# Optimization experiments

Measured on AMD Instinct MI355X. Metric: run time of the kernel, lower is better.

## Reference

```python
import jax, jax.numpy as jnp
import numpy as np

VOCAB = 50257   # vocab_size
BASE = 64       # base_dim
DD = 64         # domain_dim (hidden width of each tiny domain MLP)
ND = 16         # number of grown domains (<= max_domains=30)
B, S = 16, 8192
CORR_SCALE = 0.1  # correction scale from forward()


def setup_inputs() -> dict:
    key = jax.random.key(0)
    k1, k2, k3, k4, k5 = jax.random.split(key, 5)
    x = jax.random.randint(k1, (B, S), 0, VOCAB)
    # token -> domain assignment; values >= ND mean "no domain" (~half assigned)
    token_domain = jax.random.randint(k2, (VOCAB,), 0, 2 * ND)
    base_embed = jax.random.normal(k3, (VOCAB, BASE), dtype=jnp.float32) * 0.02
    W1 = jax.random.normal(k4, (ND, BASE, DD), dtype=jnp.float32) * 0.01
    W2 = jax.random.normal(k5, (ND, DD, BASE), dtype=jnp.float32) * 0.01
    return {"x": x, "token_domain": token_domain,
            "base_embed": base_embed, "W1": W1, "W2": W2}


def reference(x, token_domain, base_embed, W1, W2):
    # h: [B, S, BASE] base embedding lookup
    h = base_embed[x]
    d = token_domain[x]  # [B, S] domain id per token; >= ND -> unassigned
    out = h
    # Loop over the small fixed set of domains (MoE-style combine).
    # Each domain: Linear(no bias) -> exact GELU -> Linear(no bias), scaled by 0.1,
    # added only where the token belongs to that domain.
    for i in range(ND):
        hid = jax.nn.gelu(jnp.einsum('bsc,cd->bsd', h, W1[i]), approximate=False)
        corr = jnp.einsum('bsd,dc->bsc', hid, W2[i])
        out = out + jnp.where((d == i)[..., None], CORR_SCALE * corr, 0.0)
    return out
```

## Files before the change

kernel.cpp:

```cpp
#include <hip/hip_runtime.h>
#include <hip/hip_bf16.h>

#define VOCABSZ 50257
#define BASEDIM 64
#define ND 16
#define NTOK (16 * 8192)
#define NBLK_PER_DOM 32

typedef __attribute__((ext_vector_type(8))) short short8;
typedef __attribute__((ext_vector_type(4))) float f32x4;

__device__ __forceinline__ short f2bf(float f) {
    union { float f; unsigned u; } v; v.f = f;
    unsigned r = (v.u + 0x7FFFu + ((v.u >> 16) & 1u)) >> 16;
    return (short)r;
}

__global__ __launch_bounds__(256) void k_bucket_base(
    const int* __restrict__ x, const int* __restrict__ tdom,
    const float* __restrict__ emb, float* __restrict__ out,
    int* __restrict__ g_cnt, int* __restrict__ bucket, int cap)
{
    __shared__ int sm_d[256];
    __shared__ int sm_x[256];
    __shared__ int sm_cnt[ND];
    __shared__ int sm_base[ND];

    const int lt = threadIdx.x;
    const int t0 = blockIdx.x * 256;
    const int t  = t0 + lt;

    if (lt < ND) sm_cnt[lt] = 0;
    __syncthreads();

    const int xt = x[t];
    const int d  = tdom[xt];
    sm_x[lt] = xt;
    sm_d[lt] = d;
    int pos = -1;
    if (d < ND) pos = atomicAdd(&sm_cnt[d], 1);
    __syncthreads();

    if (lt < ND) sm_base[lt] = atomicAdd(&g_cnt[lt], sm_cnt[lt]);
    __syncthreads();

    if (d < ND) {
        const int gp = sm_base[d] + pos;
        if (gp < cap) bucket[d * cap + gp] = t;
    }

    const int g = lt >> 4, l16 = lt & 15;
    const float4* embv = (const float4*)emb;
    float4* outv = (float4*)out;
    #pragma unroll
    for (int it = 0; it < 16; ++it) {
        const int li = it * 16 + g;
        if (sm_d[li] >= ND) {
            outv[(size_t)(t0 + li) * 16 + l16] =
                embv[(size_t)sm_x[li] * 16 + l16];
        }
    }
}

__global__ __launch_bounds__(256) void k_domain(
    const int* __restrict__ x, const float* __restrict__ emb,
    const float* __restrict__ W1, const float* __restrict__ W2,
    const int* __restrict__ g_cnt, const int* __restrict__ bucket,
    int cap, float* __restrict__ out)
{
    const int blk   = blockIdx.x;
    const int d     = blk >> 5;
    const int chunk = blk & 31;
    int cnt = g_cnt[d];
    if (cnt > cap) cnt = cap;

    const int wave = threadIdx.x >> 6;
    const int lane = threadIdx.x & 63;
    const int kr   = (lane >> 4) * 8;
    const int nco  = lane & 15;

    const float* w1 = W1 + (size_t)d * 4096;
    const float* w2 = W2 + (size_t)d * 4096;
    short8 fw1[8], fw2[8];
    #pragma unroll
    for (int kt = 0; kt < 2; ++kt) {
        #pragma unroll
        for (int nt = 0; nt < 4; ++nt) {
            short8 a, b;
            #pragma unroll
            for (int i = 0; i < 8; ++i) {
                const int k = kt * 32 + kr + i;
                const int n = nt * 16 + nco;
                a[i] = f2bf(w1[k * 64 + n]);
                b[i] = f2bf(w2[k * 64 + n]);
            }
            fw1[kt * 4 + nt] = a;
            fw2[kt * 4 + nt] = b;
        }
    }

    __shared__ __align__(16) short sm_hid[4][16 * 72];
    short* hidb = &sm_hid[wave][0];

    const int* buck = bucket + (size_t)d * cap;

    for (int base = chunk * 64; base < cnt; base += NBLK_PER_DOM * 64) {
        const int s0 = base + wave * 16;
        int rem = cnt - s0;
        if (rem <= 0) continue;
        if (rem > 16) rem = 16;

        const int m_idx = s0 + (nco < rem ? nco : rem - 1);
        const int tm = buck[m_idx];
        const float* hrow = emb + (size_t)x[tm] * 64;
        short8 ha[2];
        #pragma unroll
        for (int kt = 0; kt < 2; ++kt) {
            const float4* hv = (const float4*)(hrow + kt * 32 + kr);
            const float4 p = hv[0], q = hv[1];
            short8 t;
            t[0] = f2bf(p.x); t[1] = f2bf(p.y); t[2] = f2bf(p.z); t[3] = f2bf(p.w);
            t[4] = f2bf(q.x); t[5] = f2bf(q.y); t[6] = f2bf(q.z); t[7] = f2bf(q.w);
            ha[kt] = t;
        }

        f32x4 acc[4];
        #pragma unroll
        for (int nt = 0; nt < 4; ++nt) {
            acc[nt] = (f32x4){0.f, 0.f, 0.f, 0.f};
            acc[nt] = __builtin_amdgcn_mfma_f32_16x16x32_bf16(ha[0], fw1[nt],     acc[nt], 0, 0, 0);
            acc[nt] = __builtin_amdgcn_mfma_f32_16x16x32_bf16(ha[1], fw1[4 + nt], acc[nt], 0, 0, 0);
        }

        #pragma unroll
        for (int nt = 0; nt < 4; ++nt) {
            #pragma unroll
            for (int i = 0; i < 4; ++i) {
                const float v  = acc[nt][i];
                const float gv = 0.5f * v * (1.0f + erff(v * 0.70710678118f));
                const int  mm  = (lane >> 4) * 4 + i;
                const int  c   = nt * 16 + nco;
                hidb[mm * 72 + c] = f2bf(gv);
            }
        }
        asm volatile("s_waitcnt lgkmcnt(0)" ::: "memory");

        short8 pa[2];
        #pragma unroll
        for (int kt = 0; kt < 2; ++kt)
            pa[kt] = *(const short8*)&hidb[(lane & 15) * 72 + kt * 32 + kr];

        f32x4 acc2[4];
        #pragma unroll
        for (int nt = 0; nt < 4; ++nt) {
            acc2[nt] = (f32x4){0.f, 0.f, 0.f, 0.f};
            acc2[nt] = __builtin_amdgcn_mfma_f32_16x16x32_bf16(pa[0], fw2[nt],     acc2[nt], 0, 0, 0);
            acc2[nt] = __builtin_amdgcn_mfma_f32_16x16x32_bf16(pa[1], fw2[4 + nt], acc2[nt], 0, 0, 0);
        }

        #pragma unroll
        for (int i = 0; i < 4; ++i) {
            const int mm = (lane >> 4) * 4 + i;
            if (mm < rem) {
                const int tt = buck[s0 + mm];
                const float* hr = emb + (size_t)x[tt] * 64;
                float* orow = out + (size_t)tt * 64;
                #pragma unroll
                for (int nt = 0; nt < 4; ++nt) {
                    const int c = nt * 16 + nco;
                    orow[c] = hr[c] + 0.1f * acc2[nt][i];
                }
            }
        }
    }
}

extern "C" void kernel_launch(void* const* d_in, const int* in_sizes, int n_in,
                              void* d_out, int out_size, void* d_ws, size_t ws_size,
                              hipStream_t stream) {
    const int*   x    = (const int*)d_in[0];
    const int*   tdom = (const int*)d_in[1];
    const float* emb  = (const float*)d_in[2];
    const float* W1   = (const float*)d_in[3];
    const float* W2   = (const float*)d_in[4];
    float* out = (float*)d_out;

    int* g_cnt  = (int*)d_ws;
    int* bucket = g_cnt + 16;
    size_t avail_ints = (ws_size > 64) ? (ws_size - 64) / 4 : 0;
    long cap_l = (long)(avail_ints / ND);
    int cap = (cap_l > NTOK) ? NTOK : (int)cap_l;

    hipMemsetAsync(d_ws, 0, ND * sizeof(int), stream);
    hipLaunchKernelGGL(k_bucket_base, dim3(NTOK / 256), dim3(256), 0, stream,
                       x, tdom, emb, out, g_cnt, bucket, cap);
    hipLaunchKernelGGL(k_domain, dim3(ND * NBLK_PER_DOM), dim3(256), 0, stream,
                       x, emb, W1, W2, g_cnt, bucket, cap, out);
}
```

Measured before the change: 111.7 us.

## Precompute corrected embedding table per vocab entry, then gather per token

Moves bucketing and the domain MLP correction from per-token to per-vocabulary-entry, writing a corrected embedding table into workspace, then gathers rows by token id. This removes redundant MLP work for repeated tokens and shrinks the bucket arrays. It adds a third kernel launch, a table of about 13MB in workspace, and a fixed per-domain capacity that no longer checks the workspace size.

```diff
diff --git a/kernel.cpp b/kernel.cpp
--- a/kernel.cpp
+++ b/kernel.cpp
@@ -5,7 +5,8 @@
 #define BASEDIM 64
 #define ND 16
 #define NTOK (16 * 8192)
-#define NBLK_PER_DOM 32
+#define CAP 4096
+#define NBLK2 8
 
 typedef __attribute__((ext_vector_type(8))) short short8;
 typedef __attribute__((ext_vector_type(4))) float f32x4;
@@ -16,26 +17,23 @@
     return (short)r;
 }
 
-__global__ __launch_bounds__(256) void k_bucket_base(
-    const int* __restrict__ x, const int* __restrict__ tdom,
-    const float* __restrict__ emb, float* __restrict__ out,
-    int* __restrict__ g_cnt, int* __restrict__ bucket, int cap)
+__global__ __launch_bounds__(256) void k_vbucket(
+    const int* __restrict__ tdom, const float* __restrict__ emb,
+    float* __restrict__ table, int* __restrict__ g_cnt, int* __restrict__ bucket)
 {
     __shared__ int sm_d[256];
-    __shared__ int sm_x[256];
     __shared__ int sm_cnt[ND];
     __shared__ int sm_base[ND];
 
     const int lt = threadIdx.x;
-    const int t0 = blockIdx.x * 256;
-    const int t  = t0 + lt;
+    const int v0 = blockIdx.x * 256;
+    const int v  = v0 + lt;
 
     if (lt < ND) sm_cnt[lt] = 0;
     __syncthreads();
 
-    const int xt = x[t];
-    const int d  = tdom[xt];
-    sm_x[lt] = xt;
+    int d = 0x7fffffff;
+    if (v < VOCABSZ) d = tdom[v];
     sm_d[lt] = d;
     int pos = -1;
     if (d < ND) pos = atomicAdd(&sm_cnt[d], 1);
@@ -46,33 +44,31 @@
 
     if (d < ND) {
         const int gp = sm_base[d] + pos;
-        if (gp < cap) bucket[d * cap + gp] = t;
+        if (gp < CAP) bucket[d * CAP + gp] = v;
     }
 
     const int g = lt >> 4, l16 = lt & 15;
-    const float4* embv = (const float4*)emb;
-    float4* outv = (float4*)out;
+    const float4* ev = (const float4*)emb;
+    float4* tv = (float4*)table;
     #pragma unroll
     for (int it = 0; it < 16; ++it) {
         const int li = it * 16 + g;
-        if (sm_d[li] >= ND) {
-            outv[(size_t)(t0 + li) * 16 + l16] =
-                embv[(size_t)sm_x[li] * 16 + l16];
-        }
-    }
-}
-
-__global__ __launch_bounds__(256) void k_domain(
-    const int* __restrict__ x, const float* __restrict__ emb,
-    const float* __restrict__ W1, const float* __restrict__ W2,
-    const int* __restrict__ g_cnt, const int* __restrict__ bucket,
-    int cap, float* __restrict__ out)
+        const int vv = v0 + li;
+        if (vv < VOCABSZ && sm_d[li] >= ND)
+            tv[(size_t)vv * 16 + l16] = ev[(size_t)vv * 16 + l16];
+    }
+}
+
+__global__ __launch_bounds__(256) void k_vcorrect(
+    const float* __restrict__ emb, const float* __restrict__ W1,
+    const float* __restrict__ W2, const int* __restrict__ g_cnt,
+    const int* __restrict__ bucket, float* __restrict__ table)
 {
     const int blk   = blockIdx.x;
-    const int d     = blk >> 5;
-    const int chunk = blk & 31;
+    const int d     = blk / NBLK2;
+    const int chunk = blk % NBLK2;
     int cnt = g_cnt[d];
-    if (cnt > cap) cnt = cap;
+    if (cnt > CAP) cnt = CAP;
 
     const int wave = threadIdx.x >> 6;
     const int lane = threadIdx.x & 63;
@@ -102,17 +98,17 @@
     __shared__ __align__(16) short sm_hid[4][16 * 72];
     short* hidb = &sm_hid[wave][0];
 
-    const int* buck = bucket + (size_t)d * cap;
-
-    for (int base = chunk * 64; base < cnt; base += NBLK_PER_DOM * 64) {
+    const int* buck = bucket + (size_t)d * CAP;
+
+    for (int base = chunk * 64; base < cnt; base += NBLK2 * 64) {
         const int s0 = base + wave * 16;
         int rem = cnt - s0;
         if (rem <= 0) continue;
         if (rem > 16) rem = 16;
 
         const int m_idx = s0 + (nco < rem ? nco : rem - 1);
-        const int tm = buck[m_idx];
-        const float* hrow = emb + (size_t)x[tm] * 64;
+        const int vm = buck[m_idx];
+        const float* hrow = emb + (size_t)vm * 64;
         short8 ha[2];
         #pragma unroll
         for (int kt = 0; kt < 2; ++kt) {
@@ -162,17 +158,28 @@
         for (int i = 0; i < 4; ++i) {
             const int mm = (lane >> 4) * 4 + i;
             if (mm < rem) {
-                const int tt = buck[s0 + mm];
-                const float* hr = emb + (size_t)x[tt] * 64;
-                float* orow = out + (size_t)tt * 64;
+                const int vv = buck[s0 + mm];
+                const float* hr = emb + (size_t)vv * 64;
+                float* trow = table + (size_t)vv * 64;
                 #pragma unroll
                 for (int nt = 0; nt < 4; ++nt) {
                     const int c = nt * 16 + nco;
-                    orow[c] = hr[c] + 0.1f * acc2[nt][i];
+                    trow[c] = hr[c] + 0.1f * acc2[nt][i];
                 }
             }
         }
     }
+}
+
+__global__ __launch_bounds__(256) void k_gather(
+    const int* __restrict__ x, const float* __restrict__ table,
+    float* __restrict__ out)
+{
+    const int idx = blockIdx.x * 256 + threadIdx.x;
+    const int row = idx >> 4, l16 = idx & 15;
+    const int xr  = x[row];
+    ((float4*)out)[(size_t)row * 16 + l16] =
+        ((const float4*)table)[(size_t)xr * 16 + l16];
 }
 
 extern "C" void kernel_launch(void* const* d_in, const int* in_sizes, int n_in,
@@ -185,15 +192,15 @@
     const float* W2   = (const float*)d_in[4];
     float* out = (float*)d_out;
 
-    int* g_cnt  = (int*)d_ws;
-    int* bucket = g_cnt + 16;
-    size_t avail_ints = (ws_size > 64) ? (ws_size - 64) / 4 : 0;
-    long cap_l = (long)(avail_ints / ND);
-    int cap = (cap_l > NTOK) ? NTOK : (int)cap_l;
+    int*   g_cnt  = (int*)d_ws;
+    int*   bucket = (int*)((char*)d_ws + 1024);
+    float* table  = (float*)((char*)d_ws + (1u << 20));
 
     hipMemsetAsync(d_ws, 0, ND * sizeof(int), stream);
-    hipLaunchKernelGGL(k_bucket_base, dim3(NTOK / 256), dim3(256), 0, stream,
-                       x, tdom, emb, out, g_cnt, bucket, cap);
-    hipLaunchKernelGGL(k_domain, dim3(ND * NBLK_PER_DOM), dim3(256), 0, stream,
-                       x, emb, W1, W2, g_cnt, bucket, cap, out);
-}
+    hipLaunchKernelGGL(k_vbucket, dim3((VOCABSZ + 255) / 256), dim3(256), 0,
+                       stream, tdom, emb, table, g_cnt, bucket);
+    hipLaunchKernelGGL(k_vcorrect, dim3(ND * NBLK2), dim3(256), 0, stream,
+                       emb, W1, W2, g_cnt, bucket, table);
+    hipLaunchKernelGGL(k_gather, dim3(NTOK * 16 / 256), dim3(256), 0, stream,
+                       x, table, out);
+}
```

After: 116.6 us. +4.3%, slower.
